# Optimization experiments

Measured on AMD Instinct MI355X. Metric: run time of the kernel, lower is better.

The kernel has to match this reference:

```python
import jax, jax.numpy as jnp
import numpy as np

# DeBut factor chain: each entry is [output_size, input_size, row, col, diag]
R_SHAPES = [[2048, 2048, 4, 4, 1],
            [2048, 2048, 8, 8, 4],
            [1024, 2048, 4, 8, 32],
            [512, 1024, 8, 16, 64]]
K = 4          # kernel_size
PAD = 0        # padding
IN_SIZE = 512 * K  # input_channel * kernel_size = 2048
NUM_PARAMS = sum(o * c for (o, _, _, c, _) in R_SHAPES)  # 40960


def setup_inputs() -> dict:
    key = jax.random.key(0)
    k1, k2, k3 = jax.random.split(key, 3)
    x = jax.random.normal(k1, (16, 512, 2048), dtype=jnp.float32)
    twiddle = jax.random.normal(k2, (NUM_PARAMS,), dtype=jnp.float32) * (1.0 / np.sqrt(2.0))
    bound = 1.0 / np.sqrt(IN_SIZE)
    bias = jax.random.uniform(k3, (512,), dtype=jnp.float32, minval=-bound, maxval=bound)
    return {"x": x, "twiddle": twiddle, "bias": bias}


def _pre_process(x):
    # x: (B, C, L) -> im2col rows (B*l_out, K*C), matching torch unfold + permute(0,3,2,1)
    B, C, L = x.shape
    l_out = L + 2 * PAD - (K - 1)
    xp = jnp.pad(x, ((0, 0), (0, 0), (PAD, PAD)))
    # (B, C, K, l_out): window offset axis (small fixed loop over K)
    win = jnp.stack([xp[:, :, i:i + l_out] for i in range(K)], axis=2)
    # -> (B, l_out, K, C) -> (B*l_out, K*C)
    return win.transpose(0, 3, 2, 1).reshape(B * l_out, K * C), l_out


def _debut_mult(rows, twiddle):
    # rows: (N, in_size); chain of block-diagonal butterfly factors
    out = rows
    p = 0
    for (osz, isz, row, col, diag) in R_SHAPES:
        g = isz // (col * diag)          # number of blocks
        n_p = col * osz
        # t: (g, row, col, diag)
        t = twiddle[p:p + n_p].reshape(g, diag, row, col).transpose(0, 2, 3, 1)
        xr = out.reshape(-1, g, col, diag)
        # contract over col within each block: (N, g, row, diag)
        out = jnp.einsum('grcd,bgcd->bgrd', t, xr)
        p += n_p
    return out.reshape(out.shape[0], -1)  # (N, out_size)


def reference(x, twiddle, bias):
    B, C, L = x.shape
    rows, l_out = _pre_process(x)
    out = _debut_mult(rows, twiddle) + bias
    # (B, l_out, out_channel) -> (B, out_channel, l_out)
    return out.reshape(B, l_out, -1).transpose(0, 2, 1)
```

## Files before the change

### kernel.cpp

```cpp
#include <hip/hip_runtime.h>

#define L_IN   2048
#define C_IN   512
#define L_OUT  2045
#define XT_PAD 21
#define CS     520
#define GP2S   524

typedef short short8 __attribute__((ext_vector_type(8)));
typedef float float4v __attribute__((ext_vector_type(4)));

__device__ __forceinline__ unsigned short bf16r(float f) {
    unsigned u = __float_as_uint(f);
    unsigned r = (u + 0x7FFFu + ((u >> 16) & 1u)) >> 16;
    return (unsigned short)r;
}

__device__ __forceinline__ unsigned bf16pk(float lo, float hi) {
    return (unsigned)bf16r(lo) | ((unsigned)bf16r(hi) << 16);
}

#define BAR() do { asm volatile("s_waitcnt lgkmcnt(0)" ::: "memory"); \
                   __builtin_amdgcn_s_barrier(); } while (0)

__global__ __launch_bounds__(256)
void build_wf(const float* __restrict__ tw, unsigned short* __restrict__ W21f,
              unsigned short* __restrict__ W43f) {
    int id = blockIdx.x * 256 + threadIdx.x;
    if (id < 65536) {
        int p = id & 7, lane = (id >> 3) & 63, oh = (id >> 9) & 1, g = id >> 10;
        int a = oh * 16 + (lane & 15);
        int e = ((lane >> 4) & 3) * 8 + p;
        int r2 = a >> 2, d2 = a & 3, c2 = e >> 2, c1 = e & 3;
        float v = tw[8192 + ((g * 4 + d2) * 8 + r2) * 8 + c2]
                * tw[(g * 8 + c2) * 16 + d2 * 4 + c1];
        W21f[id] = bf16r(v);
    } else if (id < 98304) {
        int id2 = id - 65536;
        int p = id2 & 7, lane = (id2 >> 3) & 63, kh = (id2 >> 9) & 1, s = id2 >> 10;
        int u = lane & 15;
        int w = kh * 32 + ((lane >> 4) & 3) * 8 + p;
        int r4 = u >> 1, hi = u & 1, d4 = hi * 32 + s, p2 = w >> 3, c3 = w & 7;
        float v = 0.f;
        #pragma unroll
        for (int lo = 0; lo < 2; ++lo)
            v += tw[32768 + (d4 * 8 + r4) * 16 + (2 * p2 + lo)]
               * tw[24576 + ((p2 * 32 + s) * 4 + (2 * lo + hi)) * 8 + c3];
        W43f[id2] = bf16r(v);
    }
}

__global__ __launch_bounds__(512, 4)
void debut_fused_mfma(const unsigned short* __restrict__ W21f,
                      const unsigned short* __restrict__ W43f,
                      const float* __restrict__ x,
                      const float* __restrict__ bias, float* __restrict__ out) {
    __shared__ unsigned short xtile[35 * CS];
    __shared__ unsigned int   out2[16 * GP2S];

    const int bid = blockIdx.x;
    const int swz = (bid & 7) * 128 + (bid >> 3);
    const int lt = swz & 63, b = swz >> 6;
    const int l0 = lt * 32;
    const int t = threadIdx.x;
    const int lane = t & 63, wv = t >> 6;
    const int lr = lane & 15, lh = lane >> 4;

    const float* xb = x + (size_t)b * C_IN * L_IN;

    short8 wf[8];
    #pragma unroll
    for (int k2 = 0; k2 < 2; ++k2)
        #pragma unroll
        for (int q = 0; q < 2; ++q)
            #pragma unroll
            for (int oh = 0; oh < 2; ++oh) {
                const int g = (wv * 2 + k2) * 2 + q;
                wf[k2 * 4 + q * 2 + oh] =
                    *(const short8*)(W21f + ((size_t)(g * 2 + oh) * 64 + lane) * 8);
            }
    short8 wa[4][2];
    #pragma unroll
    for (int si = 0; si < 4; ++si) {
        int s = wv * 4 + si;
        wa[si][0] = *(const short8*)(W43f + ((size_t)(s * 2 + 0) * 64 + lane) * 8);
        wa[si][1] = *(const short8*)(W43f + ((size_t)(s * 2 + 1) * 64 + lane) * 8);
    }

    {
        const int lq = t & 3, ccq = t >> 2;
        #pragma unroll
        for (int half = 0; half < 2; ++half)
            #pragma unroll
            for (int pass = 0; pass < 4; ++pass) {
                int cc = pass * 128 + ccq;
                int lrow = half * 16 + lq * 4;
                float4 v = *reinterpret_cast<const float4*>(xb + (size_t)cc * L_IN + l0 + lrow);
                int base = lrow * CS + cc;
                xtile[base         ] = bf16r(v.x);
                xtile[base + CS    ] = bf16r(v.y);
                xtile[base + 2 * CS] = bf16r(v.z);
                xtile[base + 3 * CS] = bf16r(v.w);
            }
        int cc = t;
        int lx = l0 + 32; if (lx > L_IN - 4) lx = L_IN - 4;
        float4 v = *reinterpret_cast<const float4*>(xb + (size_t)cc * L_IN + lx);
        int base = 32 * CS + cc;
        xtile[base         ] = bf16r(v.x);
        xtile[base + CS    ] = bf16r(v.y);
        xtile[base + 2 * CS] = bf16r(v.z);
    }

    BAR();

#define STAGE_A(LH, PH)                                                                  \
    do {                                                                                 \
        const int koff = 2 * (PH) + (wv >> 2);                                           \
        const unsigned short* xrow = &xtile[((LH) * 16 + lr + koff) * CS + lh * 8];      \
        _Pragma("unroll")                                                                \
        for (int k2 = 0; k2 < 2; ++k2) {                                                 \
            const int gp2 = wv * 2 + k2;                                                 \
            float4v accA[2][2];                                                          \
            _Pragma("unroll")                                                            \
            for (int q = 0; q < 2; ++q) {                                                \
                const int gl = gp2 * 2 + q;                                              \
                short8 vfrag = *(const short8*)(xrow + (gl & 15) * 32);                  \
                _Pragma("unroll")                                                        \
                for (int oh = 0; oh < 2; ++oh) {                                         \
                    float4v z = {};                                                      \
                    accA[q][oh] = __builtin_amdgcn_mfma_f32_16x16x32_bf16(               \
                        vfrag, wf[k2 * 4 + q * 2 + oh], z, 0, 0, 0);                     \
                }                                                                        \
            }                                                                            \
            _Pragma("unroll")                                                            \
            for (int oh = 0; oh < 2; ++oh) {                                             \
                const int a = oh * 16 + lr;                                              \
                uint4 w;                                                                 \
                w.x = bf16pk(accA[0][oh][0], accA[1][oh][0]);                            \
                w.y = bf16pk(accA[0][oh][1], accA[1][oh][1]);                            \
                w.z = bf16pk(accA[0][oh][2], accA[1][oh][2]);                            \
                w.w = bf16pk(accA[0][oh][3], accA[1][oh][3]);                            \
                *(uint4*)&out2[gp2 * GP2S + a * 16 + lh * 4] = w;                        \
            }                                                                            \
        }                                                                                \
    } while (0)

#define STAGE_B(ACC, PH)                                                                 \
    do {                                                                                 \
        _Pragma("unroll")                                                                \
        for (int si = 0; si < 4; ++si) {                                                 \
            const int s = wv * 4 + si;                                                   \
            const int rb = s * 16 + lr;                                                  \
            uint4 uw;                                                                    \
            uw.x = out2[(lh * 4 + 0) * GP2S + rb];                                       \
            uw.y = out2[(lh * 4 + 1) * GP2S + rb];                                       \
            uw.z = out2[(lh * 4 + 2) * GP2S + rb];                                       \
            uw.w = out2[(lh * 4 + 3) * GP2S + rb];                                       \
            short8 bb = *reinterpret_cast<short8*>(&uw);                                 \
            ACC[si] = __builtin_amdgcn_mfma_f32_16x16x32_bf16(wa[si][PH], bb, ACC[si], 0, 0, 0); \
        }                                                                                \
    } while (0)

#define LOADWF(PH)                                                                       \
    do {                                                                                 \
        _Pragma("unroll")                                                                \
        for (int k2 = 0; k2 < 2; ++k2)                                                   \
            _Pragma("unroll")                                                            \
            for (int q = 0; q < 2; ++q)                                                  \
                _Pragma("unroll")                                                        \
                for (int oh = 0; oh < 2; ++oh) {                                         \
                    const int g = (PH) * 32 + (wv * 2 + k2) * 2 + q;                     \
                    wf[k2 * 4 + q * 2 + oh] =                                            \
                        *(const short8*)(W21f + ((size_t)(g * 2 + oh) * 64 + lane) * 8); \
                }                                                                        \
    } while (0)

    float4v accB0[4] = {};
    float4v accB1[4] = {};

    STAGE_A(0, 0);
    BAR();
    STAGE_B(accB0, 0);
    BAR();
    STAGE_A(1, 0);
    BAR();
    LOADWF(1);
    STAGE_B(accB1, 0);
    BAR();

    STAGE_A(0, 1);
    BAR();
    STAGE_B(accB0, 1);
    BAR();
    STAGE_A(1, 1);
    BAR();
    STAGE_B(accB1, 1);

#undef STAGE_A
#undef STAGE_B
#undef LOADWF

    const int lpos0 = l0 + lr;
    const int lpos1 = l0 + 16 + lr;
    #pragma unroll
    for (int si = 0; si < 4; ++si) {
        const int s = wv * 4 + si;
        #pragma unroll
        for (int i = 0; i < 4; ++i) {
            int o4 = s + 32 * (lh * 4 + i);
            size_t ro = (size_t)(b * 512 + o4) * L_OUT;
            float bv = bias[o4];
            if (lpos0 < L_OUT) out[ro + lpos0] = accB0[si][i] + bv;
            if (lpos1 < L_OUT) out[ro + lpos1] = accB1[si][i] + bv;
        }
    }
}

__global__ __launch_bounds__(256)
void debut_fused_kernel(const float* __restrict__ x,
                        const float* __restrict__ tw,
                        const float* __restrict__ bias,
                        float* __restrict__ out)
{
    __shared__ float xt[C_IN * XT_PAD];
    __shared__ float bufA[2048];
    __shared__ float bufB[2048];
    const int tile = blockIdx.x, b = blockIdx.y;
    const int l0 = tile * 16;
    const int tid = threadIdx.x;
    const float* xb = x + (size_t)b * C_IN * L_IN;
    for (int idx = tid; idx < C_IN * 19; idx += 256) {
        int c = idx / 19, ll = idx - c * 19, l = l0 + ll;
        xt[c * XT_PAD + ll] = (l < L_IN) ? xb[c * L_IN + l] : 0.0f;
    }
    __syncthreads();
    const float* t1 = tw; const float* t2 = tw + 8192;
    const float* t3 = tw + 24576; const float* t4 = tw + 32768;
    for (int rr = 0; rr < 16; ++rr) {
        const int l = l0 + rr;
        if (l >= L_OUT) break;
        #pragma unroll
        for (int i = 0; i < 8; ++i) {
            int o = tid + 256 * i, gb = o >> 2, k = gb >> 7, cb = (gb & 127) << 2;
            const float4 tq = *reinterpret_cast<const float4*>(t1 + o * 4);
            const float* xp = &xt[cb * XT_PAD + rr + k];
            bufA[o] = tq.x * xp[0] + tq.y * xp[XT_PAD] + tq.z * xp[2 * XT_PAD] + tq.w * xp[3 * XT_PAD];
        }
        __syncthreads();
        #pragma unroll
        for (int i = 0; i < 8; ++i) {
            int o = tid + 256 * i, gb = o >> 5, r = (o >> 2) & 7, d = o & 3;
            const float* tp = t2 + (((gb << 2) + d) * 8 + r) * 8;
            const float* ip = &bufA[(gb << 5) + d];
            float acc = 0.0f;
            #pragma unroll
            for (int c = 0; c < 8; ++c) acc += tp[c] * ip[c << 2];
            bufB[o] = acc;
        }
        __syncthreads();
        #pragma unroll
        for (int i = 0; i < 4; ++i) {
            int o = tid + 256 * i, gb = o >> 7, r = (o >> 5) & 3, d = o & 31;
            const float* tp = t3 + (((gb << 5) + d) * 4 + r) * 8;
            const float* ip = &bufB[(gb << 8) + d];
            float acc = 0.0f;
            #pragma unroll
            for (int c = 0; c < 8; ++c) acc += tp[c] * ip[c << 5];
            bufA[o] = acc;
        }
        __syncthreads();
        #pragma unroll
        for (int i = 0; i < 2; ++i) {
            int o = tid + 256 * i, r = o >> 6, d = o & 63;
            const float* tp = t4 + ((d << 3) + r) * 16;
            float acc = 0.0f;
            #pragma unroll
            for (int c = 0; c < 16; ++c) acc += tp[c] * bufA[(c << 6) + d];
            out[((size_t)(b * 512 + o)) * L_OUT + l] = acc + bias[o];
        }
        __syncthreads();
    }
}

extern "C" void kernel_launch(void* const* d_in, const int* in_sizes, int n_in,
                              void* d_out, int out_size, void* d_ws, size_t ws_size,
                              hipStream_t stream) {
    const float* x    = (const float*)d_in[0];
    const float* tw   = (const float*)d_in[1];
    const float* bias = (const float*)d_in[2];
    float* out = (float*)d_out;

    const size_t W21_B = 65536 * 2;
    const size_t W43_B = 32768 * 2;

    if (ws_size < W21_B + W43_B) {
        dim3 grid(128, 16);
        debut_fused_kernel<<<grid, dim3(256), 0, stream>>>(x, tw, bias, out);
        return;
    }

    unsigned short* W21f = (unsigned short*)d_ws;
    unsigned short* W43f = (unsigned short*)((char*)d_ws + W21_B);

    build_wf<<<dim3(384), dim3(256), 0, stream>>>(tw, W21f, W43f);
    debut_fused_mfma<<<dim3(1024), dim3(512), 0, stream>>>(W21f, W43f, x, bias, out);
}
```

Measured before the change: 45.37 us.

## Split x tile staging so the second half loads during the first compute stage

The x tile load into LDS is split in two. All global loads are issued up front, but only rows 0-16 are converted and written before the first barrier. Rows 17-34 are held in registers and written to LDS after the first STAGE_A/STAGE_B pass, so their global-load latency overlaps with MFMA work. Bias values are also preloaded into registers early rather than read in the output loop. The cost is roughly 36 extra live VGPRs under a tight launch bound, which risks spills or lower occupancy.

```diff
diff --git a/kernel.cpp b/kernel.cpp
--- a/kernel.cpp
+++ b/kernel.cpp
@@ -65,8 +65,20 @@
     const int t = threadIdx.x;
     const int lane = t & 63, wv = t >> 6;
     const int lr = lane & 15, lh = lane >> 4;
+    const int lq = t & 3, ccq = t >> 2;
 
     const float* xb = x + (size_t)b * C_IN * L_IN;
+
+    float4 xh0[4];
+    #pragma unroll
+    for (int pass = 0; pass < 4; ++pass)
+        xh0[pass] = *reinterpret_cast<const float4*>(xb + (size_t)(pass * 128 + ccq) * L_IN + l0 + lq * 4);
+    float r16[4];
+    if (lq == 0) {
+        #pragma unroll
+        for (int pass = 0; pass < 4; ++pass)
+            r16[pass] = xb[(size_t)(pass * 128 + ccq) * L_IN + l0 + 16];
+    }
 
     short8 wf[8];
     #pragma unroll
@@ -87,28 +99,36 @@
         wa[si][1] = *(const short8*)(W43f + ((size_t)(s * 2 + 1) * 64 + lane) * 8);
     }
 
+    float4 xh1[4];
+    #pragma unroll
+    for (int pass = 0; pass < 4; ++pass)
+        xh1[pass] = *reinterpret_cast<const float4*>(xb + (size_t)(pass * 128 + ccq) * L_IN + l0 + 16 + lq * 4);
+    float4 xt4;
     {
-        const int lq = t & 3, ccq = t >> 2;
-        #pragma unroll
-        for (int half = 0; half < 2; ++half)
-            #pragma unroll
-            for (int pass = 0; pass < 4; ++pass) {
-                int cc = pass * 128 + ccq;
-                int lrow = half * 16 + lq * 4;
-                float4 v = *reinterpret_cast<const float4*>(xb + (size_t)cc * L_IN + l0 + lrow);
-                int base = lrow * CS + cc;
-                xtile[base         ] = bf16r(v.x);
-                xtile[base + CS    ] = bf16r(v.y);
-                xtile[base + 2 * CS] = bf16r(v.z);
-                xtile[base + 3 * CS] = bf16r(v.w);
-            }
-        int cc = t;
         int lx = l0 + 32; if (lx > L_IN - 4) lx = L_IN - 4;
-        float4 v = *reinterpret_cast<const float4*>(xb + (size_t)cc * L_IN + lx);
-        int base = 32 * CS + cc;
-        xtile[base         ] = bf16r(v.x);
-        xtile[base + CS    ] = bf16r(v.y);
-        xtile[base + 2 * CS] = bf16r(v.z);
+        xt4 = *reinterpret_cast<const float4*>(xb + (size_t)t * L_IN + lx);
+    }
+
+    float bv[4][4];
+    #pragma unroll
+    for (int si = 0; si < 4; ++si)
+        #pragma unroll
+        for (int i = 0; i < 4; ++i)
+            bv[si][i] = bias[wv * 4 + si + 32 * (lh * 4 + i)];
+
+    #pragma unroll
+    for (int pass = 0; pass < 4; ++pass) {
+        int cc = pass * 128 + ccq;
+        int base = (lq * 4) * CS + cc;
+        xtile[base         ] = bf16r(xh0[pass].x);
+        xtile[base + CS    ] = bf16r(xh0[pass].y);
+        xtile[base + 2 * CS] = bf16r(xh0[pass].z);
+        xtile[base + 3 * CS] = bf16r(xh0[pass].w);
+    }
+    if (lq == 0) {
+        #pragma unroll
+        for (int pass = 0; pass < 4; ++pass)
+            xtile[16 * CS + pass * 128 + ccq] = bf16r(r16[pass]);
     }
 
     BAR();
@@ -181,6 +201,20 @@
     STAGE_A(0, 0);
     BAR();
     STAGE_B(accB0, 0);
+
+    #pragma unroll
+    for (int pass = 0; pass < 4; ++pass) {
+        int cc = pass * 128 + ccq;
+        int base = (16 + lq * 4) * CS + cc;
+        if (lq != 0) xtile[base] = bf16r(xh1[pass].x);
+        xtile[base + CS    ] = bf16r(xh1[pass].y);
+        xtile[base + 2 * CS] = bf16r(xh1[pass].z);
+        xtile[base + 3 * CS] = bf16r(xh1[pass].w);
+    }
+    xtile[32 * CS + t] = bf16r(xt4.x);
+    xtile[33 * CS + t] = bf16r(xt4.y);
+    xtile[34 * CS + t] = bf16r(xt4.z);
+
     BAR();
     STAGE_A(1, 0);
     BAR();
@@ -209,9 +243,8 @@
         for (int i = 0; i < 4; ++i) {
             int o4 = s + 32 * (lh * 4 + i);
             size_t ro = (size_t)(b * 512 + o4) * L_OUT;
-            float bv = bias[o4];
-            if (lpos0 < L_OUT) out[ro + lpos0] = accB0[si][i] + bv;
-            if (lpos1 < L_OUT) out[ro + lpos1] = accB1[si][i] + bv;
+            if (lpos0 < L_OUT) out[ro + lpos0] = accB0[si][i] + bv[si][i];
+            if (lpos1 < L_OUT) out[ro + lpos1] = accB1[si][i] + bv[si][i];
         }
     }
 }
```

Result: slower. 65.39 us (+44.1%).
